# Kernel optimization log

Hardware: AMD Instinct MI355X
Metric: run time of the kernel (lower is better)

The kernel has to match this reference:

```python
import jax, jax.numpy as jnp
import numpy as np

SIZE = 4096
N_ITER = 10
TEMP = 0.1


def setup_inputs() -> dict:
    key = jax.random.key(0)
    kx, kw = jax.random.split(key)
    x = jax.random.normal(kx, (4, 2048, SIZE), dtype=jnp.float32)
    weight = jax.random.normal(kw, (SIZE, SIZE), dtype=jnp.float32)
    r_prev = jnp.zeros((SIZE, 1), dtype=jnp.float32)
    c_prev = jnp.zeros((1, SIZE), dtype=jnp.float32)
    return {"x": x, "weight": weight, "r_prev": r_prev, "c_prev": c_prev}


def reference(x, weight, r_prev, c_prev):
    Q = weight / TEMP  # [S, S]

    def body(i, rc):
        r, c = rc
        r = -jax.nn.logsumexp(Q + c, axis=1, keepdims=True)  # [S, 1]
        c = -jax.nn.logsumexp(Q + r, axis=0, keepdims=True)  # [1, S]
        return (r, c)

    r, c = jax.lax.fori_loop(0, N_ITER, body, (r_prev, c_prev))
    P = jnp.exp(Q + r + c)  # doubly-stochastic-ish [S, S]
    # F.linear(x, P) == x @ P.T
    return jnp.einsum('btd,od->bto', x, P)
```

## Files before the change

kernel.cpp:

```cpp
#include <hip/hip_runtime.h>


#define L2E 1.44269504088896340736f

typedef __attribute__((ext_vector_type(8))) short bf16x8;
typedef __attribute__((ext_vector_type(4))) float f32x4;

__device__ __forceinline__ unsigned short f2bf(float x) {
  unsigned u = __float_as_uint(x);
  u += 0x7fffu + ((u >> 16) & 1u);
  return (unsigned short)(u >> 16);
}
__device__ __forceinline__ float bf2f(short x) {
  return __uint_as_float(((unsigned)(unsigned short)x) << 16);
}

__global__ void prep_e(const float* __restrict__ W, unsigned short* __restrict__ E) {
  const int row = blockIdx.x;
  const int t = threadIdx.x;
  const float* wp = W + ((size_t)row << 12);
  float v[16];
  float m = -3.4e38f;
#pragma unroll
  for (int ch = 0; ch < 4; ++ch) {
    float4 wv = *(const float4*)(wp + ch * 1024 + t * 4);
    float a0 = 10.f * wv.x, a1 = 10.f * wv.y, a2 = 10.f * wv.z, a3 = 10.f * wv.w;
    v[ch * 4 + 0] = a0; v[ch * 4 + 1] = a1; v[ch * 4 + 2] = a2; v[ch * 4 + 3] = a3;
    m = fmaxf(m, fmaxf(fmaxf(a0, a1), fmaxf(a2, a3)));
  }
#pragma unroll
  for (int off = 32; off > 0; off >>= 1) m = fmaxf(m, __shfl_xor(m, off));
  __shared__ float sm[4];
  if ((t & 63) == 0) sm[t >> 6] = m;
  __syncthreads();
  m = fmaxf(fmaxf(sm[0], sm[1]), fmaxf(sm[2], sm[3]));
  unsigned short* ep = E + ((size_t)row << 12);
#pragma unroll
  for (int ch = 0; ch < 4; ++ch) {
    ushort4 o;
    o.x = f2bf(exp2f((v[ch * 4 + 0] - m) * L2E));
    o.y = f2bf(exp2f((v[ch * 4 + 1] - m) * L2E));
    o.z = f2bf(exp2f((v[ch * 4 + 2] - m) * L2E));
    o.w = f2bf(exp2f((v[ch * 4 + 3] - m) * L2E));
    *(ushort4*)(ep + ch * 1024 + t * 4) = o;
  }
}

__global__ void transpose_bf(const unsigned short* __restrict__ E,
                             unsigned short* __restrict__ ET) {
  __shared__ unsigned short tile[64][66];
  const int t = threadIdx.x;
  const int r = t >> 3;
  const int c8 = (t & 7) << 3;
  const size_t i0 = (size_t)blockIdx.y << 6;
  const size_t j0 = (size_t)blockIdx.x << 6;
#pragma unroll
  for (int h = 0; h < 2; ++h) {
    bf16x8 vv = *(const bf16x8*)(E + (i0 + h * 32 + r) * 4096 + j0 + c8);
#pragma unroll
    for (int e = 0; e < 8; ++e) tile[h * 32 + r][c8 + e] = (unsigned short)vv[e];
  }
  __syncthreads();
#pragma unroll
  for (int h = 0; h < 2; ++h) {
    bf16x8 vv;
#pragma unroll
    for (int e = 0; e < 8; ++e) vv[e] = (short)tile[c8 + e][h * 32 + r];
    *(bf16x8*)(ET + (j0 + h * 32 + r) * 4096 + i0 + c8) = vv;
  }
}

__global__ void init_u(const float* __restrict__ c_prev, float* __restrict__ u) {
  const int i = blockIdx.x * 256 + threadIdx.x;
  u[i] = exp2f(c_prev[i] * L2E);
}

__global__ void recip_mv(const unsigned short* __restrict__ M,
                         const float* __restrict__ uin, float* __restrict__ vout) {
  const int t = threadIdx.x;
  const int l = t & 63, w = t >> 6;
  const int row = (blockIdx.x << 2) + w;
  const unsigned short* mp = M + ((size_t)row << 12);
  float s = 0.f;
#pragma unroll
  for (int ch = 0; ch < 8; ++ch) {
    const int j = (ch << 9) + (l << 3);
    bf16x8 e = *(const bf16x8*)(mp + j);
    const float4 u0 = *(const float4*)(uin + j);
    const float4 u1 = *(const float4*)(uin + j + 4);
    s = fmaf(bf2f(e[0]), u0.x, s);
    s = fmaf(bf2f(e[1]), u0.y, s);
    s = fmaf(bf2f(e[2]), u0.z, s);
    s = fmaf(bf2f(e[3]), u0.w, s);
    s = fmaf(bf2f(e[4]), u1.x, s);
    s = fmaf(bf2f(e[5]), u1.y, s);
    s = fmaf(bf2f(e[6]), u1.z, s);
    s = fmaf(bf2f(e[7]), u1.w, s);
  }
#pragma unroll
  for (int off = 32; off > 0; off >>= 1) s += __shfl_xor(s, off);
  if (l == 0) vout[row] = 1.f / s;
}

__global__ void scale_x(const float* __restrict__ X, const float* __restrict__ u,
                        unsigned short* __restrict__ Y) {
  const size_t idx = ((size_t)blockIdx.x * 256 + threadIdx.x) * 4;
  const int col = (int)(idx & 4095);
  float4 xv = *(const float4*)(X + idx);
  float4 uu = *(const float4*)(u + col);
  ushort4 o;
  o.x = f2bf(xv.x * uu.x);
  o.y = f2bf(xv.y * uu.y);
  o.z = f2bf(xv.z * uu.z);
  o.w = f2bf(xv.w * uu.w);
  *(ushort4*)(Y + idx) = o;
}

__global__ __launch_bounds__(256) void gemm_bt(const unsigned short* __restrict__ A,
                                               const unsigned short* __restrict__ B,
                                               const float* __restrict__ vscale,
                                               float* __restrict__ C) {
  __shared__ unsigned short As[128 * 32];
  __shared__ unsigned short Bs[128 * 32];
  int pid = blockIdx.x;
  pid = (pid & 7) * 256 + (pid >> 3);
  const int g = pid >> 8;
  const int rem = pid & 255;
  const int bm = (g << 3) + (rem & 7);
  const int bn = rem >> 3;
  const int m0 = bm << 7;
  const int n0 = bn << 7;
  const int t = threadIdx.x;
  const int l = t & 63;
  const int w = t >> 6;
  const int wr = w >> 1, wc = w & 1;
  f32x4 acc[4][4] = {};
  const int srow = l >> 2;
  const int scol = (l & 3) << 3;
  const unsigned short* Ab = A + ((size_t)m0 << 12);
  const unsigned short* Bb = B + ((size_t)n0 << 12);
  const int lrow = l & 15;
  const int lk = (l >> 4) << 3;

  for (int k0 = 0; k0 < 4096; k0 += 32) {
#pragma unroll
    for (int p = 0; p < 2; ++p) {
      const int rb = (p << 2) + w;
      const unsigned short* ga = Ab + (size_t)(rb * 16 + srow) * 4096 + k0 + scol;
      const unsigned short* gb = Bb + (size_t)(rb * 16 + srow) * 4096 + k0 + scol;
      __builtin_amdgcn_global_load_lds((const __attribute__((address_space(1))) void*)ga,
                                       (__attribute__((address_space(3))) void*)(As + rb * 512),
                                       16, 0, 0);
      __builtin_amdgcn_global_load_lds((const __attribute__((address_space(1))) void*)gb,
                                       (__attribute__((address_space(3))) void*)(Bs + rb * 512),
                                       16, 0, 0);
    }
    __syncthreads();
    bf16x8 af[4], bfr[4];
#pragma unroll
    for (int i = 0; i < 4; ++i) {
      af[i]  = *(const bf16x8*)(As + ((wr << 6) + (i << 4) + lrow) * 32 + lk);
      bfr[i] = *(const bf16x8*)(Bs + ((wc << 6) + (i << 4) + lrow) * 32 + lk);
    }
#pragma unroll
    for (int i = 0; i < 4; ++i)
#pragma unroll
      for (int j = 0; j < 4; ++j)
        acc[i][j] = __builtin_amdgcn_mfma_f32_16x16x32_bf16(af[i], bfr[j], acc[i][j], 0, 0, 0);
    __syncthreads();
  }

  const int crow = (l >> 4) << 2;
  const int ccol = l & 15;
#pragma unroll
  for (int j = 0; j < 4; ++j) {
    const int colj = n0 + (wc << 6) + (j << 4) + ccol;
    const float vs = vscale[colj];
#pragma unroll
    for (int i = 0; i < 4; ++i)
#pragma unroll
      for (int q = 0; q < 4; ++q) {
        const int rowi = m0 + (wr << 6) + (i << 4) + crow + q;
        C[((size_t)rowi << 12) + colj] = acc[i][j][q] * vs;
      }
  }
}

extern "C" void kernel_launch(void* const* d_in, const int* in_sizes, int n_in,
                              void* d_out, int out_size, void* d_ws, size_t ws_size,
                              hipStream_t stream) {
  const float* x      = (const float*)d_in[0];
  const float* weight = (const float*)d_in[1];
  const float* c_prev = (const float*)d_in[3];
  float* out = (float*)d_out;

  char* ws = (char*)d_ws;
  float* u = (float*)ws;
  float* v = (float*)(ws + (16 << 10));
  unsigned short* E  = (unsigned short*)(ws + (64 << 10));
  unsigned short* ET = E + (size_t)4096 * 4096;
  unsigned short* xb = ET;

  prep_e<<<4096, 256, 0, stream>>>(weight, E);
  transpose_bf<<<dim3(64, 64), 256, 0, stream>>>(E, ET);
  init_u<<<16, 256, 0, stream>>>(c_prev, u);

  for (int it = 0; it < 10; ++it) {
    recip_mv<<<1024, 256, 0, stream>>>(E, u, v);
    recip_mv<<<1024, 256, 0, stream>>>(ET, v, u);
  }

  scale_x<<<32768, 256, 0, stream>>>(x, u, xb);

  gemm_bt<<<2048, 256, 0, stream>>>(xb, E, v, out);
}
```

Before: 516.5 us.

## Rewrite GEMM as 256x256 tile, 8-wave kernel with 4-stage LDS pipeline

The bf16 GEMM now uses 256x256 output tiles per 512-thread block, with 8 waves each computing a 128x64 sub-tile. Operand tiles are loaded directly into LDS through a 4-buffer, 3-deep prefetch ring, with explicit vmcnt waits, barriers and s_setprio around the MFMA bursts. LDS reads use an XOR swizzle to avoid bank conflicts. This is meant to raise arithmetic intensity and hide global load latency behind MFMA work, at the cost of 128KB of LDS per block, one block per CU and a hand-tuned wait schedule that is fragile.

```diff
diff --git a/kernel.cpp b/kernel.cpp
--- a/kernel.cpp
+++ b/kernel.cpp
@@ -116,73 +116,114 @@
   *(ushort4*)(Y + idx) = o;
 }
 
-__global__ __launch_bounds__(256) void gemm_bt(const unsigned short* __restrict__ A,
+__global__ __launch_bounds__(512) void gemm_bt(const unsigned short* __restrict__ A,
                                                const unsigned short* __restrict__ B,
                                                const float* __restrict__ vscale,
                                                float* __restrict__ C) {
-  __shared__ unsigned short As[128 * 32];
-  __shared__ unsigned short Bs[128 * 32];
-  int pid = blockIdx.x;
-  pid = (pid & 7) * 256 + (pid >> 3);
-  const int g = pid >> 8;
-  const int rem = pid & 255;
-  const int bm = (g << 3) + (rem & 7);
-  const int bn = rem >> 3;
-  const int m0 = bm << 7;
-  const int n0 = bn << 7;
+  __shared__ unsigned short lds[65536];
   const int t = threadIdx.x;
   const int l = t & 63;
   const int w = t >> 6;
-  const int wr = w >> 1, wc = w & 1;
-  f32x4 acc[4][4] = {};
-  const int srow = l >> 2;
-  const int scol = (l & 3) << 3;
-  const unsigned short* Ab = A + ((size_t)m0 << 12);
-  const unsigned short* Bb = B + ((size_t)n0 << 12);
-  const int lrow = l & 15;
-  const int lk = (l >> 4) << 3;
-
-  for (int k0 = 0; k0 < 4096; k0 += 32) {
-#pragma unroll
-    for (int p = 0; p < 2; ++p) {
-      const int rb = (p << 2) + w;
-      const unsigned short* ga = Ab + (size_t)(rb * 16 + srow) * 4096 + k0 + scol;
-      const unsigned short* gb = Bb + (size_t)(rb * 16 + srow) * 4096 + k0 + scol;
-      __builtin_amdgcn_global_load_lds((const __attribute__((address_space(1))) void*)ga,
-                                       (__attribute__((address_space(3))) void*)(As + rb * 512),
-                                       16, 0, 0);
-      __builtin_amdgcn_global_load_lds((const __attribute__((address_space(1))) void*)gb,
-                                       (__attribute__((address_space(3))) void*)(Bs + rb * 512),
-                                       16, 0, 0);
-    }
-    __syncthreads();
-    bf16x8 af[4], bfr[4];
-#pragma unroll
-    for (int i = 0; i < 4; ++i) {
-      af[i]  = *(const bf16x8*)(As + ((wr << 6) + (i << 4) + lrow) * 32 + lk);
-      bfr[i] = *(const bf16x8*)(Bs + ((wc << 6) + (i << 4) + lrow) * 32 + lk);
-    }
+  const int wm = w >> 2, wn = w & 3;
+
+  int pid = blockIdx.x;
+  pid = (pid & 7) * 64 + (pid >> 3);
+  const int grp = pid >> 6;
+  const int rem = pid & 63;
+  const int bm = (grp << 2) + (rem & 3);
+  const int bn = rem >> 2;
+  const int m0 = bm << 8;
+  const int n0 = bn << 8;
+
+  const int ca = (((t & 3) ^ ((t >> 2) & 3)) << 3);
+  const unsigned short* gA = A + (size_t)(m0 + (t >> 2)) * 4096 + ca;
+  const unsigned short* gB = B + (size_t)(n0 + (t >> 2)) * 4096 + ca;
+
+  const int xc = (((l >> 4) ^ (l & 3)) << 3);
+  const int aOff = (wm * 128 + (l & 15)) * 32 + xc;
+  const int bOff = (wn * 64 + (l & 15)) * 32 + xc;
+
+  auto stageA = [&](int kt) {
+    const int b = kt & 3;
+    const unsigned short* g = gA + (size_t)kt * 32;
+#pragma unroll
+    for (int ra = 0; ra < 2; ++ra)
+      __builtin_amdgcn_global_load_lds(
+          (const __attribute__((address_space(1))) void*)(g + (size_t)ra * 524288),
+          (__attribute__((address_space(3))) void*)((char*)lds + b * 16384 + ra * 8192 + w * 1024),
+          16, 0, 0);
+  };
+  auto stageB = [&](int kt) {
+    const int b = kt & 3;
+    const unsigned short* g = gB + (size_t)kt * 32;
+#pragma unroll
+    for (int ra = 0; ra < 2; ++ra)
+      __builtin_amdgcn_global_load_lds(
+          (const __attribute__((address_space(1))) void*)(g + (size_t)ra * 524288),
+          (__attribute__((address_space(3))) void*)((char*)lds + 65536 + b * 16384 + ra * 8192 + w * 1024),
+          16, 0, 0);
+  };
+
+  f32x4 acc[8][4] = {};
+
+  stageA(0); stageB(0);
+  stageA(1); stageB(1);
+  stageA(2); stageB(2);
+  asm volatile("s_waitcnt vmcnt(8)" ::: "memory");
+  __builtin_amdgcn_s_barrier();
+
+  for (int kt = 0; kt < 128; ++kt) {
+    const int buf = kt & 3;
+    const unsigned short* aL = lds + buf * 8192 + aOff;
+    const unsigned short* bL = lds + 32768 + buf * 8192 + bOff;
+    bf16x8 afr[4], bfr[4];
+
+#pragma unroll
+    for (int i = 0; i < 4; ++i) afr[i] = *(const bf16x8*)(aL + i * 512);
+#pragma unroll
+    for (int j = 0; j < 4; ++j) bfr[j] = *(const bf16x8*)(bL + j * 512);
+    if (kt < 125) stageA(kt + 3);
+    __builtin_amdgcn_s_barrier();
+    __builtin_amdgcn_s_setprio(1);
 #pragma unroll
     for (int i = 0; i < 4; ++i)
 #pragma unroll
       for (int j = 0; j < 4; ++j)
-        acc[i][j] = __builtin_amdgcn_mfma_f32_16x16x32_bf16(af[i], bfr[j], acc[i][j], 0, 0, 0);
-    __syncthreads();
+        acc[i][j] = __builtin_amdgcn_mfma_f32_16x16x32_bf16(afr[i], bfr[j], acc[i][j], 0, 0, 0);
+    __builtin_amdgcn_s_setprio(0);
+    __builtin_amdgcn_s_barrier();
+
+#pragma unroll
+    for (int i = 0; i < 4; ++i) afr[i] = *(const bf16x8*)(aL + (4 + i) * 512);
+    if (kt < 125) stageB(kt + 3);
+    __builtin_amdgcn_s_barrier();
+    __builtin_amdgcn_s_setprio(1);
+#pragma unroll
+    for (int i = 0; i < 4; ++i)
+#pragma unroll
+      for (int j = 0; j < 4; ++j)
+        acc[4 + i][j] = __builtin_amdgcn_mfma_f32_16x16x32_bf16(afr[i], bfr[j], acc[4 + i][j], 0, 0, 0);
+    __builtin_amdgcn_s_setprio(0);
+
+    if (kt < 125)        asm volatile("s_waitcnt vmcnt(8)" ::: "memory");
+    else if (kt == 125)  asm volatile("s_waitcnt vmcnt(4)" ::: "memory");
+    else if (kt == 126)  asm volatile("s_waitcnt vmcnt(0)" ::: "memory");
+    __builtin_amdgcn_s_barrier();
   }
 
   const int crow = (l >> 4) << 2;
   const int ccol = l & 15;
 #pragma unroll
   for (int j = 0; j < 4; ++j) {
-    const int colj = n0 + (wc << 6) + (j << 4) + ccol;
+    const int colj = n0 + (wn << 6) + (j << 4) + ccol;
     const float vs = vscale[colj];
 #pragma unroll
-    for (int i = 0; i < 4; ++i)
-#pragma unroll
-      for (int q = 0; q < 4; ++q) {
-        const int rowi = m0 + (wr << 6) + (i << 4) + crow + q;
-        C[((size_t)rowi << 12) + colj] = acc[i][j][q] * vs;
-      }
+    for (int i = 0; i < 8; ++i) {
+      const int rowi = m0 + (wm << 7) + (i << 4) + crow;
+#pragma unroll
+      for (int q = 0; q < 4; ++q)
+        C[((size_t)(rowi + q) << 12) + colj] = acc[i][j][q] * vs;
+    }
   }
 }
 
@@ -212,5 +253,5 @@
 
   scale_x<<<32768, 256, 0, stream>>>(x, u, xb);
 
-  gemm_bt<<<2048, 256, 0, stream>>>(xb, E, v, out);
-}
+  gemm_bt<<<512, 512, 0, stream>>>(xb, E, v, out);
+}
```

Result: faster. 459.5 us (-11.0%).
